# Kernel optimization log

Measured on AMD Instinct MI355X. Metric: run time of the kernel, lower is better.

Reference implementation:

```python
import jax, jax.numpy as jnp
import numpy as np

NUM_HEADS = 12  # from init_kwargs


def setup_inputs() -> dict:
    key = jax.random.key(0)
    k1, k2, k3 = jax.random.split(key, 3)
    B, N, C = 8, 4096, 768
    x = jax.random.normal(k1, (B, N, C), dtype=jnp.float32)
    qkv_w = jax.random.normal(k2, (3 * C, C), dtype=jnp.float32) * (C ** -0.5)
    proj_w = jax.random.normal(k3, (C, C), dtype=jnp.float32) * (C ** -0.5)
    proj_b = jnp.zeros((C,), dtype=jnp.float32)
    return {"x": x, "qkv_w": qkv_w, "proj_w": proj_w, "proj_b": proj_b}


def reference(x, qkv_w, proj_w, proj_b):
    B, N, C = x.shape
    H = NUM_HEADS
    hd = C // H
    h = w = int(round(N ** 0.5))  # spatial grid, N = h*w
    # fused qkv projection (q, k are produced but never consumed, as in source)
    qkv = jnp.einsum('bnc,dc->bnd', x, qkv_w)          # [B, N, 3C]
    qkv = qkv.reshape(B, N, 3, H, hd)
    v = qkv[:, :, 2].transpose(0, 2, 1, 3)             # [B, H, N, hd]
    v2d = v.reshape(B, H, h, w, hd)
    # fft2 over spatial dims; concat(real, imag) then slice[:hd] == real part
    v_real = jnp.fft.fft2(v2d.astype(jnp.float32), axes=(2, 3)).real
    out = v_real.reshape(B, H, N, hd).transpose(0, 2, 1, 3).reshape(B, N, C)
    return jnp.einsum('bnc,dc->bnd', out, proj_w) + proj_b
```

## Files before the change

### kernel.cpp

```cpp
#include <hip/hip_runtime.h>
#include <hip/hip_bf16.h>


typedef __bf16 bf16x8 __attribute__((ext_vector_type(8)));
typedef __bf16 bf16x4 __attribute__((ext_vector_type(4)));
typedef float f32x4 __attribute__((ext_vector_type(4)));
typedef float f32x16 __attribute__((ext_vector_type(16)));
typedef unsigned short ushort_t;
typedef unsigned int uint_t;

typedef __attribute__((address_space(3))) unsigned int lds_u32;
typedef __attribute__((address_space(1))) unsigned int glob_u32;

__device__ __forceinline__ void gl_lds16(const void* g, void* l) {
  __builtin_amdgcn_global_load_lds((const glob_u32*)g, (lds_u32*)l, 16, 0, 0);
}

__device__ __forceinline__ ushort_t f2bf(float f) {
  union { __hip_bfloat16 h; ushort_t s; } cv;
  cv.h = __float2bfloat16(f);
  return cv.s;
}

__device__ __forceinline__ bf16x8 ld_frag(const ushort_t* p) {
  union { bf16x8 v; bf16x4 h[2]; } r;
  r.h[0] = *(const bf16x4*)p;
  r.h[1] = *(const bf16x4*)(p + 4);
  return r.v;
}

__device__ __forceinline__ bf16x8 ld_swz(const ushort_t* rowp, int D0, int sel2) {
  union { bf16x8 v; bf16x4 h[2]; } r;
  r.h[0] = *(const bf16x4*)(rowp + 2 * (D0 ^ sel2));
  r.h[1] = *(const bf16x4*)(rowp + 2 * ((D0 + 2) ^ sel2));
  return r.v;
}

__global__ __launch_bounds__(256) void prep(const float* __restrict__ P,
                                            const float* __restrict__ Q,
                                            ushort_t* __restrict__ TwA,
                                            ushort_t* __restrict__ TwB,
                                            ushort_t* __restrict__ Pb,
                                            ushort_t* __restrict__ Qb) {
  __shared__ ushort_t Ts[4608];
  const int t = threadIdx.x;
  if (blockIdx.x < 7) {
    const int id = blockIdx.x * 256 + t;
    int m, k0, sn;
    ushort_t* out;
    if (id < 768) {
      int r = id % 384, cs = id / 384;
      int l = r & 63, ks = (r >> 6) & 1, mt = r >> 7;
      m = mt * 16 + (l & 15);
      k0 = ks * 32 + (l >> 4) * 8;
      sn = cs;
      out = TwA + id * 8;
    } else {
      int j = id - 768;
      int r = j % 512, cs = j / 512;
      int l = r & 63, ks = (r >> 6) & 1, mt = (r >> 7) & 1, wm = r >> 8;
      m = wm * 32 + mt * 16 + (l & 15);
      k0 = ks * 32 + (l >> 4) * 8;
      sn = cs;
      out = TwB + j * 8;
    }
#pragma unroll
    for (int e = 0; e < 8; ++e) {
      int ph = (m * (k0 + e)) & 63;
      float a = (float)ph * 0.09817477042468104f;
      out[e] = f2bf(sn ? __sinf(a) : __cosf(a));
    }
  } else if (blockIdx.x < 151) {
    const int tile = blockIdx.x - 7;
    const int ti = tile / 12, tj = tile % 12;
    const int r0 = t >> 4, c4 = (t & 15) * 4;
#pragma unroll
    for (int rr = 0; rr < 4; ++rr) {
      const int k = ti * 64 + r0 + rr * 16;
      f32x4 v = *(const f32x4*)&Q[(size_t)(1536 + k) * 768 + tj * 64 + c4];
#pragma unroll
      for (int j = 0; j < 4; ++j)
        Ts[(c4 + j) * 72 + r0 + rr * 16] = f2bf(v[j]);
    }
    __syncthreads();
    const int co = t >> 2, kq = (t & 3) * 16;
    uint4 v0 = *(const uint4*)&Ts[co * 72 + kq];
    uint4 v1 = *(const uint4*)&Ts[co * 72 + kq + 8];
    ushort_t* dst = Qb + (size_t)(tj * 64 + co) * 768 + ti * 64 + kq;
    *(uint4*)&dst[0] = v0;
    *(uint4*)&dst[8] = v1;
  } else {
    const int cid = blockIdx.x - 151;
    const size_t off = (size_t)cid * 2048 + t * 8;
    f32x4 f0 = *(const f32x4*)&P[off];
    f32x4 f1 = *(const f32x4*)&P[off + 4];
    union { ushort_t u[8]; uint4 v; } pk;
#pragma unroll
    for (int j = 0; j < 4; ++j) { pk.u[j] = f2bf(f0[j]); pk.u[4 + j] = f2bf(f1[j]); }
    *(uint4*)&Pb[off] = pk.v;
  }
}

__global__ __launch_bounds__(256) void fft_a_pre(const float* __restrict__ X,
                                                 __hip_bfloat16* __restrict__ Ar,
                                                 __hip_bfloat16* __restrict__ Ai,
                                                 const ushort_t* __restrict__ TwA) {
  __shared__ ushort_t smem[9728];
  ushort_t* Xs = smem;
  ushort_t* Ep = smem;
  const int t = threadIdx.x;
  const int c0 = blockIdx.x * 128;
  const int w = t >> 6, l = t & 63;
  const int lm = l & 15, lq = l >> 4;
  const int s = blockIdx.y;
  const float* src = X + (size_t)s * 64 * 768 + c0;
  const bf16x8* twa = (const bf16x8*)TwA;
  bf16x8 afc[3][2], afs[3][2];
#pragma unroll
  for (int mt = 0; mt < 3; ++mt)
#pragma unroll
    for (int ks = 0; ks < 2; ++ks) {
      afc[mt][ks] = twa[mt * 128 + ks * 64 + l];
      afs[mt][ks] = twa[384 + mt * 128 + ks * 64 + l];
    }
#pragma unroll
  for (int it = 0; it < 4; ++it) {
    const int pr = it * 8 + (t >> 5);
    const int c = (t & 31) * 4;
    const float* rp = src + (size_t)(2 * pr) * 768 + c;
    f32x4 f0 = *(const f32x4*)rp;
    f32x4 f1 = *(const f32x4*)(rp + 768);
#pragma unroll
    for (int j = 0; j < 4; ++j) {
      uint_t pk = (uint_t)f2bf(f0[j]) | ((uint_t)f2bf(f1[j]) << 16);
      const int row = c + j;
      const int d = pr ^ (((row >> 4) & 7) << 1);
      *(uint_t*)&Xs[row * 68 + 2 * d] = pk;
    }
  }
  __syncthreads();
  f32x4 accr[3][2] = {}, acci[3][2] = {};
#pragma unroll
  for (int ks = 0; ks < 2; ++ks) {
    bf16x8 bf[2];
#pragma unroll
    for (int nt = 0; nt < 2; ++nt) {
      int c = w * 32 + nt * 16 + lm;
      int sel2 = ((c >> 4) & 7) << 1;
      bf[nt] = ld_swz(&Xs[c * 68], ks * 16 + lq * 4, sel2);
    }
#pragma unroll
    for (int mt = 0; mt < 3; ++mt)
#pragma unroll
      for (int nt = 0; nt < 2; ++nt) {
        accr[mt][nt] = __builtin_amdgcn_mfma_f32_16x16x32_bf16(afc[mt][ks], bf[nt], accr[mt][nt], 0, 0, 0);
        acci[mt][nt] = __builtin_amdgcn_mfma_f32_16x16x32_bf16(afs[mt][ks], bf[nt], acci[mt][nt], 0, 0, 0);
      }
  }
#pragma unroll
  for (int arr = 0; arr < 2; ++arr) {
    __syncthreads();
#pragma unroll
    for (int mt = 0; mt < 3; ++mt)
#pragma unroll
      for (int nt = 0; nt < 2; ++nt)
#pragma unroll
        for (int r = 0; r < 4; ++r) {
          int row = mt * 16 + lq * 4 + r;
          if (row <= 32) {
            int col = w * 32 + nt * 16 + lm;
            float v = arr ? acci[mt][nt][r] : accr[mt][nt][r];
            Ep[row * 136 + col] = f2bf(v);
          }
        }
    __syncthreads();
    __hip_bfloat16* dst = arr ? Ai : Ar;
#pragma unroll
    for (int it = 0; it < 3; ++it) {
      int idx = it * 256 + t;
      int row = idx >> 4, cq = (idx & 15) * 8;
      if (row <= 32) {
        uint4 v = *(const uint4*)&Ep[row * 136 + cq];
        *(uint4*)&dst[(size_t)(s * 64 + row) * 768 + c0 + cq] = v;
      }
    }
  }
}

__global__ __launch_bounds__(256) void fft_b_mfma(const __hip_bfloat16* __restrict__ Ar,
                                                  const __hip_bfloat16* __restrict__ Ai,
                                                  __hip_bfloat16* __restrict__ Xf,
                                                  const ushort_t* __restrict__ TwB,
                                                  const ushort_t* __restrict__ Pb,
                                                  const ushort_t* __restrict__ Qb,
                                                  __hip_bfloat16* __restrict__ Mb) {
  __shared__ ushort_t smem[17408];
  const int t = threadIdx.x;
  const int w = t >> 6, l = t & 63;

  if (blockIdx.y < 6) {
    ushort_t* As = smem;
    ushort_t* Bs = smem + 8192;
    const int m0 = blockIdx.y * 128;
    const int n0 = blockIdx.x * 128;
    const int wm = w & 1, wn = w >> 1;
    f32x16 acc[2][2] = {};
    const int srow = l >> 3;
    const int schunk = (l & 7) ^ srow;
    const int lr = l & 31, lh = l >> 5;
    for (int kt = 0; kt < 12; ++kt) {
      const int k0 = kt * 64;
#pragma unroll
      for (int i = 0; i < 4; ++i) {
        const int rbase = w * 32 + i * 8;
        const int row = rbase + srow;
        gl_lds16(&Pb[(size_t)(m0 + row) * 768 + k0 + schunk * 8], &As[rbase * 64]);
        gl_lds16(&Qb[(size_t)(n0 + row) * 768 + k0 + schunk * 8], &Bs[rbase * 64]);
      }
      __syncthreads();
#pragma unroll
      for (int ks = 0; ks < 4; ++ks) {
        bf16x8 af[2], bfv[2];
#pragma unroll
        for (int mt = 0; mt < 2; ++mt) {
          int row = wm * 64 + mt * 32 + lr;
          int ch = (ks * 2 + lh) ^ (lr & 7);
          af[mt] = *(const bf16x8*)&As[row * 64 + ch * 8];
        }
#pragma unroll
        for (int nt = 0; nt < 2; ++nt) {
          int row = wn * 64 + nt * 32 + lr;
          int ch = (ks * 2 + lh) ^ (lr & 7);
          bfv[nt] = *(const bf16x8*)&Bs[row * 64 + ch * 8];
        }
#pragma unroll
        for (int mt = 0; mt < 2; ++mt)
#pragma unroll
          for (int nt = 0; nt < 2; ++nt)
            acc[mt][nt] = __builtin_amdgcn_mfma_f32_32x32x16_bf16(af[mt], bfv[nt], acc[mt][nt], 0, 0, 0);
      }
      __syncthreads();
    }
#pragma unroll
    for (int nt = 0; nt < 2; ++nt) {
      const int col = n0 + wn * 64 + nt * 32 + lr;
#pragma unroll
      for (int mt = 0; mt < 2; ++mt) {
        const int rb = m0 + wm * 64 + mt * 32 + 4 * lh;
#pragma unroll
        for (int reg = 0; reg < 16; ++reg) {
          const int row = rb + (reg & 3) + 8 * (reg >> 2);
          Mb[(size_t)row * 768 + col] = __float2bfloat16(acc[mt][nt][reg]);
        }
      }
    }
    return;
  }

  ushort_t* Rs = smem;
  ushort_t* Is = smem + 8704;
  ushort_t* Ep = smem;
  const int bz = blockIdx.y - 6;
  const int b = bz / 33, k2 = bz % 33;
  const int c0 = blockIdx.x * 128;
  const ushort_t* ar = (const ushort_t*)Ar + ((size_t)(b * 64) * 64 + k2) * 768 + c0;
  const ushort_t* ai = (const ushort_t*)Ai + ((size_t)(b * 64) * 64 + k2) * 768 + c0;
  const size_t n1s = (size_t)64 * 768;
  const int wm = w & 1, wn = w >> 1;
  const int lm = l & 15, lq = l >> 4;
  const bf16x8* twb = (const bf16x8*)TwB;
  bf16x8 afc[2][2], afs[2][2];
#pragma unroll
  for (int mt = 0; mt < 2; ++mt)
#pragma unroll
    for (int ks = 0; ks < 2; ++ks) {
      afc[mt][ks] = twb[wm * 256 + mt * 128 + ks * 64 + l];
      afs[mt][ks] = twb[512 + wm * 256 + mt * 128 + ks * 64 + l];
    }
#pragma unroll
  for (int it = 0; it < 4; ++it) {
    const int pr = it * 8 + (t >> 5);
    const int c = (t & 31) * 4;
    const size_t o0 = (size_t)(2 * pr) * n1s + c;
    uint2 va = *(const uint2*)&ar[o0];
    uint2 vb = *(const uint2*)&ar[o0 + n1s];
    uint2 ia = *(const uint2*)&ai[o0];
    uint2 ib = *(const uint2*)&ai[o0 + n1s];
    uint_t rr[4], ss[4];
    rr[0] = (va.x & 0xffffu) | (vb.x << 16);
    rr[1] = (va.x >> 16) | (vb.x & 0xffff0000u);
    rr[2] = (va.y & 0xffffu) | (vb.y << 16);
    rr[3] = (va.y >> 16) | (vb.y & 0xffff0000u);
    ss[0] = (ia.x & 0xffffu) | (ib.x << 16);
    ss[1] = (ia.x >> 16) | (ib.x & 0xffff0000u);
    ss[2] = (ia.y & 0xffffu) | (ib.y << 16);
    ss[3] = (ia.y >> 16) | (ib.y & 0xffff0000u);
#pragma unroll
    for (int j = 0; j < 4; ++j) {
      const int row = c + j;
      const int d = pr ^ (((row >> 4) & 7) << 1);
      *(uint_t*)&Rs[row * 68 + 2 * d] = rr[j];
      *(uint_t*)&Is[row * 68 + 2 * d] = ss[j];
    }
  }
  __syncthreads();
  f32x4 accC[2][4] = {}, accS[2][4] = {};
#pragma unroll
  for (int ks = 0; ks < 2; ++ks) {
    bf16x8 bR[4], bI[4];
#pragma unroll
    for (int nt = 0; nt < 4; ++nt) {
      int c = wn * 64 + nt * 16 + lm;
      int sel2 = ((c >> 4) & 7) << 1;
      int D0 = ks * 16 + lq * 4;
      bR[nt] = ld_swz(&Rs[c * 68], D0, sel2);
      bI[nt] = ld_swz(&Is[c * 68], D0, sel2);
    }
#pragma unroll
    for (int mt = 0; mt < 2; ++mt)
#pragma unroll
      for (int nt = 0; nt < 4; ++nt) {
        accC[mt][nt] = __builtin_amdgcn_mfma_f32_16x16x32_bf16(afc[mt][ks], bR[nt], accC[mt][nt], 0, 0, 0);
        accS[mt][nt] = __builtin_amdgcn_mfma_f32_16x16x32_bf16(afs[mt][ks], bI[nt], accS[mt][nt], 0, 0, 0);
      }
  }
  const int nout = (k2 >= 1 && k2 <= 31) ? 2 : 1;
  for (int o = 0; o < nout; ++o) {
    __syncthreads();
#pragma unroll
    for (int mt = 0; mt < 2; ++mt)
#pragma unroll
      for (int nt = 0; nt < 4; ++nt)
#pragma unroll
        for (int r = 0; r < 4; ++r) {
          int row = wm * 32 + mt * 16 + lq * 4 + r;
          int col = wn * 64 + nt * 16 + lm;
          float v = o ? (accC[mt][nt][r] + accS[mt][nt][r])
                      : (accC[mt][nt][r] - accS[mt][nt][r]);
          Ep[row * 136 + col] = f2bf(v);
        }
    __syncthreads();
    const int k2o = o ? (64 - k2) : k2;
#pragma unroll
    for (int it = 0; it < 4; ++it) {
      int idx = it * 256 + t;
      int k1 = idx >> 4, cq = (idx & 15) * 8;
      uint4 v = *(const uint4*)&Ep[k1 * 136 + cq];
      *(uint4*)&Xf[((size_t)b * 4096 + k1 * 64 + k2o) * 768 + c0 + cq] = v;
    }
  }
}

__global__ __launch_bounds__(256) void gemm_bt(const __hip_bfloat16* __restrict__ A,
                                               const __hip_bfloat16* __restrict__ B,
                                               const float* __restrict__ bias,
                                               float* __restrict__ C) {
  __shared__ ushort_t As[128 * 64];
  __shared__ ushort_t Bs[128 * 64];
  const int t = threadIdx.x, w = t >> 6, l = t & 63;
  const int L = blockIdx.x + blockIdx.y * 6;
  const int s = L >> 3, xcd = L & 7;
  const int n0 = (s % 6) * 128;
  const int m0 = ((s / 6) * 8 + xcd) * 128;
  const int wm = w & 1, wn = w >> 1;
  f32x16 acc[2][2] = {};
  const int srow = l >> 3;
  const int schunk = (l & 7) ^ srow;
  const int lr = l & 31, lh = l >> 5;
  for (int kt = 0; kt < 12; ++kt) {
    const int k0 = kt * 64;
#pragma unroll
    for (int i = 0; i < 4; ++i) {
      const int rbase = w * 32 + i * 8;
      const int row = rbase + srow;
      gl_lds16(&A[(size_t)(m0 + row) * 768 + k0 + schunk * 8], &As[rbase * 64]);
      gl_lds16(&B[(size_t)(n0 + row) * 768 + k0 + schunk * 8], &Bs[rbase * 64]);
    }
    __syncthreads();
#pragma unroll
    for (int ks = 0; ks < 4; ++ks) {
      bf16x8 af[2], bf[2];
#pragma unroll
      for (int mt = 0; mt < 2; ++mt) {
        int row = wm * 64 + mt * 32 + lr;
        int ch = (ks * 2 + lh) ^ (lr & 7);
        af[mt] = *(const bf16x8*)&As[row * 64 + ch * 8];
      }
#pragma unroll
      for (int nt = 0; nt < 2; ++nt) {
        int row = wn * 64 + nt * 32 + lr;
        int ch = (ks * 2 + lh) ^ (lr & 7);
        bf[nt] = *(const bf16x8*)&Bs[row * 64 + ch * 8];
      }
#pragma unroll
      for (int mt = 0; mt < 2; ++mt)
#pragma unroll
        for (int nt = 0; nt < 2; ++nt)
          acc[mt][nt] = __builtin_amdgcn_mfma_f32_32x32x16_bf16(af[mt], bf[nt], acc[mt][nt], 0, 0, 0);
    }
    __syncthreads();
  }
#pragma unroll
  for (int nt = 0; nt < 2; ++nt) {
    const int col = n0 + wn * 64 + nt * 32 + lr;
    const float bv = bias[col];
#pragma unroll
    for (int mt = 0; mt < 2; ++mt) {
      const int rb = m0 + wm * 64 + mt * 32 + 4 * lh;
#pragma unroll
      for (int reg = 0; reg < 16; ++reg) {
        const int row = rb + (reg & 3) + 8 * (reg >> 2);
        C[(size_t)row * 768 + col] = acc[mt][nt][reg] + bv;
      }
    }
  }
}

extern "C" void kernel_launch(void* const* d_in, const int* in_sizes, int n_in,
                              void* d_out, int out_size, void* d_ws, size_t ws_size,
                              hipStream_t stream) {
  const float* x      = (const float*)d_in[0];
  const float* qkv_w  = (const float*)d_in[1];
  const float* proj_w = (const float*)d_in[2];
  const float* proj_b = (const float*)d_in[3];
  float* out = (float*)d_out;

  char* ws = (char*)d_ws;
  const size_t MB_BYTES = (size_t)768 * 768 * 2;
  const size_t ARR_BYTES = (size_t)8 * 4096 * 768 * 2;
  __hip_bfloat16* Mb = (__hip_bfloat16*)ws;
  __hip_bfloat16* Ar = (__hip_bfloat16*)(ws + MB_BYTES);
  __hip_bfloat16* Ai = (__hip_bfloat16*)(ws + MB_BYTES + ARR_BYTES);
  __hip_bfloat16* Xf = (__hip_bfloat16*)(ws + MB_BYTES + 2 * ARR_BYTES);
  ushort_t* Pb = (ushort_t*)(ws + MB_BYTES + 3 * ARR_BYTES);
  ushort_t* Qb = (ushort_t*)(ws + MB_BYTES + 3 * ARR_BYTES + MB_BYTES);
  ushort_t* TwA = (ushort_t*)((char*)Ar + 61440);
  ushort_t* TwB = (ushort_t*)((char*)Ar + 61440 + 12288);

  prep<<<dim3(439), 256, 0, stream>>>(proj_w, qkv_w, TwA, TwB, Pb, Qb);
  fft_a_pre<<<dim3(6, 512), 256, 0, stream>>>(x, Ar, Ai, TwA);
  fft_b_mfma<<<dim3(6, 270), 256, 0, stream>>>(Ar, Ai, Xf, TwB, Pb, Qb, Mb);
  gemm_bt<<<dim3(6, 256), 256, 0, stream>>>(Xf, Mb, proj_b, out);
}
```

Baseline: 255.2 us.

## Process two FFT slices per block in both FFT stages with overlapped epilogue

fft_a_pre now handles two 64-row slices per block, staging both into a doubled LDS buffer and writing real and imaginary outputs in one combined pass. fft_b_mfma pairs columns k2 and k2+16 per block, double-buffering LDS so the second slice's MFMA overlaps the first slice's global stores. The intent is to cut block count, launch and sync overhead and to hide epilogue latency. The cost is twice the LDS per block (about 68KB in fft_b) and more live registers, which lowers occupancy.

After: 252.0 us. About the same (-1.3%).

```diff
diff --git a/kernel.cpp b/kernel.cpp
--- a/kernel.cpp
+++ b/kernel.cpp
@@ -105,15 +105,12 @@
                                                  __hip_bfloat16* __restrict__ Ar,
                                                  __hip_bfloat16* __restrict__ Ai,
                                                  const ushort_t* __restrict__ TwA) {
-  __shared__ ushort_t smem[9728];
-  ushort_t* Xs = smem;
-  ushort_t* Ep = smem;
+  __shared__ ushort_t smem[17408];
   const int t = threadIdx.x;
   const int c0 = blockIdx.x * 128;
   const int w = t >> 6, l = t & 63;
   const int lm = l & 15, lq = l >> 4;
-  const int s = blockIdx.y;
-  const float* src = X + (size_t)s * 64 * 768 + c0;
+  const int s0 = blockIdx.y * 2;
   const bf16x8* twa = (const bf16x8*)TwA;
   bf16x8 afc[3][2], afs[3][2];
 #pragma unroll
@@ -124,64 +121,77 @@
       afs[mt][ks] = twa[384 + mt * 128 + ks * 64 + l];
     }
 #pragma unroll
-  for (int it = 0; it < 4; ++it) {
-    const int pr = it * 8 + (t >> 5);
-    const int c = (t & 31) * 4;
-    const float* rp = src + (size_t)(2 * pr) * 768 + c;
-    f32x4 f0 = *(const f32x4*)rp;
-    f32x4 f1 = *(const f32x4*)(rp + 768);
-#pragma unroll
-    for (int j = 0; j < 4; ++j) {
-      uint_t pk = (uint_t)f2bf(f0[j]) | ((uint_t)f2bf(f1[j]) << 16);
-      const int row = c + j;
-      const int d = pr ^ (((row >> 4) & 7) << 1);
-      *(uint_t*)&Xs[row * 68 + 2 * d] = pk;
+  for (int ss = 0; ss < 2; ++ss) {
+    ushort_t* Xs = smem + ss * 8704;
+    const float* src = X + (size_t)(s0 + ss) * 64 * 768 + c0;
+#pragma unroll
+    for (int it = 0; it < 4; ++it) {
+      const int pr = it * 8 + (t >> 5);
+      const int c = (t & 31) * 4;
+      const float* rp = src + (size_t)(2 * pr) * 768 + c;
+      f32x4 f0 = *(const f32x4*)rp;
+      f32x4 f1 = *(const f32x4*)(rp + 768);
+#pragma unroll
+      for (int j = 0; j < 4; ++j) {
+        uint_t pk = (uint_t)f2bf(f0[j]) | ((uint_t)f2bf(f1[j]) << 16);
+        const int row = c + j;
+        const int d = pr ^ (((row >> 4) & 7) << 1);
+        *(uint_t*)&Xs[row * 68 + 2 * d] = pk;
+      }
     }
   }
   __syncthreads();
-  f32x4 accr[3][2] = {}, acci[3][2] = {};
-#pragma unroll
-  for (int ks = 0; ks < 2; ++ks) {
-    bf16x8 bf[2];
-#pragma unroll
-    for (int nt = 0; nt < 2; ++nt) {
-      int c = w * 32 + nt * 16 + lm;
-      int sel2 = ((c >> 4) & 7) << 1;
-      bf[nt] = ld_swz(&Xs[c * 68], ks * 16 + lq * 4, sel2);
-    }
-#pragma unroll
-    for (int mt = 0; mt < 3; ++mt)
+  f32x4 accr[2][3][2] = {}, acci[2][3][2] = {};
+#pragma unroll
+  for (int ss = 0; ss < 2; ++ss) {
+    const ushort_t* Xs = smem + ss * 8704;
+#pragma unroll
+    for (int ks = 0; ks < 2; ++ks) {
+      bf16x8 bf[2];
 #pragma unroll
       for (int nt = 0; nt < 2; ++nt) {
-        accr[mt][nt] = __builtin_amdgcn_mfma_f32_16x16x32_bf16(afc[mt][ks], bf[nt], accr[mt][nt], 0, 0, 0);
-        acci[mt][nt] = __builtin_amdgcn_mfma_f32_16x16x32_bf16(afs[mt][ks], bf[nt], acci[mt][nt], 0, 0, 0);
-      }
-  }
-#pragma unroll
-  for (int arr = 0; arr < 2; ++arr) {
-    __syncthreads();
-#pragma unroll
-    for (int mt = 0; mt < 3; ++mt)
-#pragma unroll
-      for (int nt = 0; nt < 2; ++nt)
-#pragma unroll
-        for (int r = 0; r < 4; ++r) {
-          int row = mt * 16 + lq * 4 + r;
-          if (row <= 32) {
-            int col = w * 32 + nt * 16 + lm;
-            float v = arr ? acci[mt][nt][r] : accr[mt][nt][r];
-            Ep[row * 136 + col] = f2bf(v);
+        int c = w * 32 + nt * 16 + lm;
+        int sel2 = ((c >> 4) & 7) << 1;
+        bf[nt] = ld_swz(&Xs[c * 68], ks * 16 + lq * 4, sel2);
+      }
+#pragma unroll
+      for (int mt = 0; mt < 3; ++mt)
+#pragma unroll
+        for (int nt = 0; nt < 2; ++nt) {
+          accr[ss][mt][nt] = __builtin_amdgcn_mfma_f32_16x16x32_bf16(afc[mt][ks], bf[nt], accr[ss][mt][nt], 0, 0, 0);
+          acci[ss][mt][nt] = __builtin_amdgcn_mfma_f32_16x16x32_bf16(afs[mt][ks], bf[nt], acci[ss][mt][nt], 0, 0, 0);
+        }
+    }
+  }
+#pragma unroll
+  for (int ss = 0; ss < 2; ++ss) {
+    __syncthreads();
+#pragma unroll
+    for (int arr = 0; arr < 2; ++arr)
+#pragma unroll
+      for (int mt = 0; mt < 3; ++mt)
+#pragma unroll
+        for (int nt = 0; nt < 2; ++nt)
+#pragma unroll
+          for (int r = 0; r < 4; ++r) {
+            int row = mt * 16 + lq * 4 + r;
+            if (row <= 32) {
+              int col = w * 32 + nt * 16 + lm;
+              float v = arr ? acci[ss][mt][nt][r] : accr[ss][mt][nt][r];
+              smem[arr * 6528 + row * 136 + col] = f2bf(v);
+            }
           }
-        }
-    __syncthreads();
-    __hip_bfloat16* dst = arr ? Ai : Ar;
-#pragma unroll
-    for (int it = 0; it < 3; ++it) {
+    __syncthreads();
+#pragma unroll
+    for (int it = 0; it < 5; ++it) {
       int idx = it * 256 + t;
-      int row = idx >> 4, cq = (idx & 15) * 8;
-      if (row <= 32) {
-        uint4 v = *(const uint4*)&Ep[row * 136 + cq];
-        *(uint4*)&dst[(size_t)(s * 64 + row) * 768 + c0 + cq] = v;
+      if (idx < 1056) {
+        int arr = idx >= 528 ? 1 : 0;
+        int rem = idx - arr * 528;
+        int row = rem >> 4, cq = (rem & 15) * 8;
+        uint4 v = *(const uint4*)&smem[arr * 6528 + row * 136 + cq];
+        __hip_bfloat16* dst = arr ? Ai : Ar;
+        *(uint4*)&dst[(size_t)((s0 + ss) * 64 + row) * 768 + c0 + cq] = v;
       }
     }
   }
@@ -194,7 +204,7 @@
                                                   const ushort_t* __restrict__ Pb,
                                                   const ushort_t* __restrict__ Qb,
                                                   __hip_bfloat16* __restrict__ Mb) {
-  __shared__ ushort_t smem[17408];
+  __shared__ ushort_t smem[34816];
   const int t = threadIdx.x;
   const int w = t >> 6, l = t & 63;
 
@@ -257,14 +267,12 @@
     return;
   }
 
-  ushort_t* Rs = smem;
-  ushort_t* Is = smem + 8704;
-  ushort_t* Ep = smem;
   const int bz = blockIdx.y - 6;
-  const int b = bz / 33, k2 = bz % 33;
+  const int b = bz / 17, kp = bz % 17;
+  const int nk = (kp == 16) ? 1 : 2;
+  const int k2v0 = (kp == 16) ? 32 : kp;
+  const int k2v1 = kp + 16;
   const int c0 = blockIdx.x * 128;
-  const ushort_t* ar = (const ushort_t*)Ar + ((size_t)(b * 64) * 64 + k2) * 768 + c0;
-  const ushort_t* ai = (const ushort_t*)Ai + ((size_t)(b * 64) * 64 + k2) * 768 + c0;
   const size_t n1s = (size_t)64 * 768;
   const int wm = w & 1, wn = w >> 1;
   const int lm = l & 15, lq = l >> 4;
@@ -277,77 +285,117 @@
       afc[mt][ks] = twb[wm * 256 + mt * 128 + ks * 64 + l];
       afs[mt][ks] = twb[512 + wm * 256 + mt * 128 + ks * 64 + l];
     }
-#pragma unroll
-  for (int it = 0; it < 4; ++it) {
-    const int pr = it * 8 + (t >> 5);
-    const int c = (t & 31) * 4;
-    const size_t o0 = (size_t)(2 * pr) * n1s + c;
-    uint2 va = *(const uint2*)&ar[o0];
-    uint2 vb = *(const uint2*)&ar[o0 + n1s];
-    uint2 ia = *(const uint2*)&ai[o0];
-    uint2 ib = *(const uint2*)&ai[o0 + n1s];
-    uint_t rr[4], ss[4];
-    rr[0] = (va.x & 0xffffu) | (vb.x << 16);
-    rr[1] = (va.x >> 16) | (vb.x & 0xffff0000u);
-    rr[2] = (va.y & 0xffffu) | (vb.y << 16);
-    rr[3] = (va.y >> 16) | (vb.y & 0xffff0000u);
-    ss[0] = (ia.x & 0xffffu) | (ib.x << 16);
-    ss[1] = (ia.x >> 16) | (ib.x & 0xffff0000u);
-    ss[2] = (ia.y & 0xffffu) | (ib.y << 16);
-    ss[3] = (ia.y >> 16) | (ib.y & 0xffff0000u);
-#pragma unroll
-    for (int j = 0; j < 4; ++j) {
-      const int row = c + j;
-      const int d = pr ^ (((row >> 4) & 7) << 1);
-      *(uint_t*)&Rs[row * 68 + 2 * d] = rr[j];
-      *(uint_t*)&Is[row * 68 + 2 * d] = ss[j];
-    }
-  }
+
+  auto stage = [&](int kk, int k2) {
+    ushort_t* Rs = smem + kk * 17408;
+    ushort_t* Is = Rs + 8704;
+    const ushort_t* ar = (const ushort_t*)Ar + ((size_t)(b * 64) * 64 + k2) * 768 + c0;
+    const ushort_t* ai = (const ushort_t*)Ai + ((size_t)(b * 64) * 64 + k2) * 768 + c0;
+#pragma unroll
+    for (int it = 0; it < 4; ++it) {
+      const int pr = it * 8 + (t >> 5);
+      const int c = (t & 31) * 4;
+      const size_t o0 = (size_t)(2 * pr) * n1s + c;
+      uint2 va = *(const uint2*)&ar[o0];
+      uint2 vb = *(const uint2*)&ar[o0 + n1s];
+      uint2 ia = *(const uint2*)&ai[o0];
+      uint2 ib = *(const uint2*)&ai[o0 + n1s];
+      uint_t rr[4], ss_[4];
+      rr[0] = (va.x & 0xffffu) | (vb.x << 16);
+      rr[1] = (va.x >> 16) | (vb.x & 0xffff0000u);
+      rr[2] = (va.y & 0xffffu) | (vb.y << 16);
+      rr[3] = (va.y >> 16) | (vb.y & 0xffff0000u);
+      ss_[0] = (ia.x & 0xffffu) | (ib.x << 16);
+      ss_[1] = (ia.x >> 16) | (ib.x & 0xffff0000u);
+      ss_[2] = (ia.y & 0xffffu) | (ib.y << 16);
+      ss_[3] = (ia.y >> 16) | (ib.y & 0xffff0000u);
+#pragma unroll
+      for (int j = 0; j < 4; ++j) {
+        const int row = c + j;
+        const int d = pr ^ (((row >> 4) & 7) << 1);
+        *(uint_t*)&Rs[row * 68 + 2 * d] = rr[j];
+        *(uint_t*)&Is[row * 68 + 2 * d] = ss_[j];
+      }
+    }
+  };
+
+  auto do_mfma = [&](int kk, f32x4 (&aC)[2][4], f32x4 (&aS)[2][4]) {
+    const ushort_t* Rs = smem + kk * 17408;
+    const ushort_t* Is = Rs + 8704;
+#pragma unroll
+    for (int ks = 0; ks < 2; ++ks) {
+      bf16x8 bR[4], bI[4];
+#pragma unroll
+      for (int nt = 0; nt < 4; ++nt) {
+        int c = wn * 64 + nt * 16 + lm;
+        int sel2 = ((c >> 4) & 7) << 1;
+        int D0 = ks * 16 + lq * 4;
+        bR[nt] = ld_swz(&Rs[c * 68], D0, sel2);
+        bI[nt] = ld_swz(&Is[c * 68], D0, sel2);
+      }
+#pragma unroll
+      for (int mt = 0; mt < 2; ++mt)
+#pragma unroll
+        for (int nt = 0; nt < 4; ++nt) {
+          aC[mt][nt] = __builtin_amdgcn_mfma_f32_16x16x32_bf16(afc[mt][ks], bR[nt], aC[mt][nt], 0, 0, 0);
+          aS[mt][nt] = __builtin_amdgcn_mfma_f32_16x16x32_bf16(afs[mt][ks], bI[nt], aS[mt][nt], 0, 0, 0);
+        }
+    }
+  };
+
+  auto ep_write = [&](int kk, int nout, f32x4 (&aC)[2][4], f32x4 (&aS)[2][4]) {
+    ushort_t* Ep = smem + kk * 17408;
+    for (int o = 0; o < nout; ++o)
+#pragma unroll
+      for (int mt = 0; mt < 2; ++mt)
+#pragma unroll
+        for (int nt = 0; nt < 4; ++nt)
+#pragma unroll
+          for (int r = 0; r < 4; ++r) {
+            int row = wm * 32 + mt * 16 + lq * 4 + r;
+            int col = wn * 64 + nt * 16 + lm;
+            float v = o ? (aC[mt][nt][r] + aS[mt][nt][r])
+                        : (aC[mt][nt][r] - aS[mt][nt][r]);
+            Ep[o * 8704 + row * 136 + col] = f2bf(v);
+          }
+  };
+
+  auto gout = [&](int kk, int k2, int nout) {
+    const ushort_t* Ep = smem + kk * 17408;
+#pragma unroll
+    for (int it = 0; it < 8; ++it) {
+      int idx = it * 256 + t;
+      if (idx < nout * 1024) {
+        int o = idx >> 10, rem = idx & 1023;
+        int k1 = rem >> 4, cq = (rem & 15) * 8;
+        uint4 v = *(const uint4*)&Ep[o * 8704 + k1 * 136 + cq];
+        int k2o = o ? (64 - k2) : k2;
+        *(uint4*)&Xf[((size_t)b * 4096 + k1 * 64 + k2o) * 768 + c0 + cq] = v;
+      }
+    }
+  };
+
+  const int nout0 = (k2v0 >= 1 && k2v0 <= 31) ? 2 : 1;
+  stage(0, k2v0);
+  if (nk == 2) stage(1, k2v1);
   __syncthreads();
-  f32x4 accC[2][4] = {}, accS[2][4] = {};
-#pragma unroll
-  for (int ks = 0; ks < 2; ++ks) {
-    bf16x8 bR[4], bI[4];
-#pragma unroll
-    for (int nt = 0; nt < 4; ++nt) {
-      int c = wn * 64 + nt * 16 + lm;
-      int sel2 = ((c >> 4) & 7) << 1;
-      int D0 = ks * 16 + lq * 4;
-      bR[nt] = ld_swz(&Rs[c * 68], D0, sel2);
-      bI[nt] = ld_swz(&Is[c * 68], D0, sel2);
-    }
-#pragma unroll
-    for (int mt = 0; mt < 2; ++mt)
-#pragma unroll
-      for (int nt = 0; nt < 4; ++nt) {
-        accC[mt][nt] = __builtin_amdgcn_mfma_f32_16x16x32_bf16(afc[mt][ks], bR[nt], accC[mt][nt], 0, 0, 0);
-        accS[mt][nt] = __builtin_amdgcn_mfma_f32_16x16x32_bf16(afs[mt][ks], bI[nt], accS[mt][nt], 0, 0, 0);
-      }
-  }
-  const int nout = (k2 >= 1 && k2 <= 31) ? 2 : 1;
-  for (int o = 0; o < nout; ++o) {
-    __syncthreads();
-#pragma unroll
-    for (int mt = 0; mt < 2; ++mt)
-#pragma unroll
-      for (int nt = 0; nt < 4; ++nt)
-#pragma unroll
-        for (int r = 0; r < 4; ++r) {
-          int row = wm * 32 + mt * 16 + lq * 4 + r;
-          int col = wn * 64 + nt * 16 + lm;
-          float v = o ? (accC[mt][nt][r] + accS[mt][nt][r])
-                      : (accC[mt][nt][r] - accS[mt][nt][r]);
-          Ep[row * 136 + col] = f2bf(v);
-        }
-    __syncthreads();
-    const int k2o = o ? (64 - k2) : k2;
-#pragma unroll
-    for (int it = 0; it < 4; ++it) {
-      int idx = it * 256 + t;
-      int k1 = idx >> 4, cq = (idx & 15) * 8;
-      uint4 v = *(const uint4*)&Ep[k1 * 136 + cq];
-      *(uint4*)&Xf[((size_t)b * 4096 + k1 * 64 + k2o) * 768 + c0 + cq] = v;
-    }
+  {
+    f32x4 aC[2][4] = {}, aS[2][4] = {};
+    do_mfma(0, aC, aS);
+    __syncthreads();
+    ep_write(0, nout0, aC, aS);
+  }
+  __syncthreads();
+  if (nk == 2) {
+    f32x4 aC[2][4] = {}, aS[2][4] = {};
+    do_mfma(1, aC, aS);
+    gout(0, k2v0, nout0);
+    __syncthreads();
+    ep_write(1, 2, aC, aS);
+    __syncthreads();
+    gout(1, k2v1, 2);
+  } else {
+    gout(0, k2v0, nout0);
   }
 }
 
@@ -438,7 +486,7 @@
   ushort_t* TwB = (ushort_t*)((char*)Ar + 61440 + 12288);
 
   prep<<<dim3(439), 256, 0, stream>>>(proj_w, qkv_w, TwA, TwB, Pb, Qb);
-  fft_a_pre<<<dim3(6, 512), 256, 0, stream>>>(x, Ar, Ai, TwA);
-  fft_b_mfma<<<dim3(6, 270), 256, 0, stream>>>(Ar, Ai, Xf, TwB, Pb, Qb, Mb);
+  fft_a_pre<<<dim3(6, 256), 256, 0, stream>>>(x, Ar, Ai, TwA);
+  fft_b_mfma<<<dim3(6, 142), 256, 0, stream>>>(Ar, Ai, Xf, TwB, Pb, Qb, Mb);
   gemm_bt<<<dim3(6, 256), 256, 0, stream>>>(Xf, Mb, proj_b, out);
 }
```

## Compact intermediate FFT arrays to k2-major layout and merge epilogue syncs

Applied to the files above, without the earlier changes.

Stores the first-stage FFT outputs Ar/Ai in a packed [b][k2][n1] layout of 33 rows instead of strided 64-row slots. The second stage then reads contiguous 768-wide rows rather than rows strided by 64*768. Both FFT kernels now stage both epilogue outputs in shared memory at once and write them after a single barrier instead of looping with two barriers per output. Twiddle buffers move to their own workspace region. The aim is better read locality and coalescing, a smaller intermediate footprint and fewer barriers, at the cost of more shared memory live at the same time.

New measurement: 253.1 us. About the same (-0.8%).

```diff
diff --git a/kernel.cpp b/kernel.cpp
--- a/kernel.cpp
+++ b/kernel.cpp
@@ -20,13 +20,6 @@
   union { __hip_bfloat16 h; ushort_t s; } cv;
   cv.h = __float2bfloat16(f);
   return cv.s;
-}
-
-__device__ __forceinline__ bf16x8 ld_frag(const ushort_t* p) {
-  union { bf16x8 v; bf16x4 h[2]; } r;
-  r.h[0] = *(const bf16x4*)p;
-  r.h[1] = *(const bf16x4*)(p + 4);
-  return r.v;
 }
 
 __device__ __forceinline__ bf16x8 ld_swz(const ushort_t* rowp, int D0, int sel2) {
@@ -106,13 +99,12 @@
                                                  __hip_bfloat16* __restrict__ Ai,
                                                  const ushort_t* __restrict__ TwA) {
   __shared__ ushort_t smem[9728];
-  ushort_t* Xs = smem;
-  ushort_t* Ep = smem;
   const int t = threadIdx.x;
   const int c0 = blockIdx.x * 128;
   const int w = t >> 6, l = t & 63;
   const int lm = l & 15, lq = l >> 4;
   const int s = blockIdx.y;
+  const int b = s >> 6, n1 = s & 63;
   const float* src = X + (size_t)s * 64 * 768 + c0;
   const bf16x8* twa = (const bf16x8*)TwA;
   bf16x8 afc[3][2], afs[3][2];
@@ -135,7 +127,7 @@
       uint_t pk = (uint_t)f2bf(f0[j]) | ((uint_t)f2bf(f1[j]) << 16);
       const int row = c + j;
       const int d = pr ^ (((row >> 4) & 7) << 1);
-      *(uint_t*)&Xs[row * 68 + 2 * d] = pk;
+      *(uint_t*)&smem[row * 68 + 2 * d] = pk;
     }
   }
   __syncthreads();
@@ -147,7 +139,7 @@
     for (int nt = 0; nt < 2; ++nt) {
       int c = w * 32 + nt * 16 + lm;
       int sel2 = ((c >> 4) & 7) << 1;
-      bf[nt] = ld_swz(&Xs[c * 68], ks * 16 + lq * 4, sel2);
+      bf[nt] = ld_swz(&smem[c * 68], ks * 16 + lq * 4, sel2);
     }
 #pragma unroll
     for (int mt = 0; mt < 3; ++mt)
@@ -157,9 +149,9 @@
         acci[mt][nt] = __builtin_amdgcn_mfma_f32_16x16x32_bf16(afs[mt][ks], bf[nt], acci[mt][nt], 0, 0, 0);
       }
   }
-#pragma unroll
-  for (int arr = 0; arr < 2; ++arr) {
-    __syncthreads();
+  __syncthreads();
+#pragma unroll
+  for (int arr = 0; arr < 2; ++arr)
 #pragma unroll
     for (int mt = 0; mt < 3; ++mt)
 #pragma unroll
@@ -170,19 +162,20 @@
           if (row <= 32) {
             int col = w * 32 + nt * 16 + lm;
             float v = arr ? acci[mt][nt][r] : accr[mt][nt][r];
-            Ep[row * 136 + col] = f2bf(v);
+            smem[arr * 4488 + row * 136 + col] = f2bf(v);
           }
         }
-    __syncthreads();
-    __hip_bfloat16* dst = arr ? Ai : Ar;
-#pragma unroll
-    for (int it = 0; it < 3; ++it) {
-      int idx = it * 256 + t;
-      int row = idx >> 4, cq = (idx & 15) * 8;
-      if (row <= 32) {
-        uint4 v = *(const uint4*)&Ep[row * 136 + cq];
-        *(uint4*)&dst[(size_t)(s * 64 + row) * 768 + c0 + cq] = v;
-      }
+  __syncthreads();
+#pragma unroll
+  for (int it = 0; it < 5; ++it) {
+    int idx = it * 256 + t;
+    if (idx < 1056) {
+      int arr = idx >= 528 ? 1 : 0;
+      int rem = idx - arr * 528;
+      int row = rem >> 4, cq = (rem & 15) * 8;
+      uint4 v = *(const uint4*)&smem[arr * 4488 + row * 136 + cq];
+      __hip_bfloat16* dst = arr ? Ai : Ar;
+      *(uint4*)&dst[((size_t)(b * 33 + row) * 64 + n1) * 768 + c0 + cq] = v;
     }
   }
 }
@@ -259,13 +252,11 @@
 
   ushort_t* Rs = smem;
   ushort_t* Is = smem + 8704;
-  ushort_t* Ep = smem;
   const int bz = blockIdx.y - 6;
   const int b = bz / 33, k2 = bz % 33;
   const int c0 = blockIdx.x * 128;
-  const ushort_t* ar = (const ushort_t*)Ar + ((size_t)(b * 64) * 64 + k2) * 768 + c0;
-  const ushort_t* ai = (const ushort_t*)Ai + ((size_t)(b * 64) * 64 + k2) * 768 + c0;
-  const size_t n1s = (size_t)64 * 768;
+  const ushort_t* ar = (const ushort_t*)Ar + (size_t)(b * 33 + k2) * 64 * 768 + c0;
+  const ushort_t* ai = (const ushort_t*)Ai + (size_t)(b * 33 + k2) * 64 * 768 + c0;
   const int wm = w & 1, wn = w >> 1;
   const int lm = l & 15, lq = l >> 4;
   const bf16x8* twb = (const bf16x8*)TwB;
@@ -281,26 +272,26 @@
   for (int it = 0; it < 4; ++it) {
     const int pr = it * 8 + (t >> 5);
     const int c = (t & 31) * 4;
-    const size_t o0 = (size_t)(2 * pr) * n1s + c;
+    const size_t o0 = (size_t)(2 * pr) * 768 + c;
     uint2 va = *(const uint2*)&ar[o0];
-    uint2 vb = *(const uint2*)&ar[o0 + n1s];
+    uint2 vb = *(const uint2*)&ar[o0 + 768];
     uint2 ia = *(const uint2*)&ai[o0];
-    uint2 ib = *(const uint2*)&ai[o0 + n1s];
-    uint_t rr[4], ss[4];
+    uint2 ib = *(const uint2*)&ai[o0 + 768];
+    uint_t rr[4], ss_[4];
     rr[0] = (va.x & 0xffffu) | (vb.x << 16);
     rr[1] = (va.x >> 16) | (vb.x & 0xffff0000u);
     rr[2] = (va.y & 0xffffu) | (vb.y << 16);
     rr[3] = (va.y >> 16) | (vb.y & 0xffff0000u);
-    ss[0] = (ia.x & 0xffffu) | (ib.x << 16);
-    ss[1] = (ia.x >> 16) | (ib.x & 0xffff0000u);
-    ss[2] = (ia.y & 0xffffu) | (ib.y << 16);
-    ss[3] = (ia.y >> 16) | (ib.y & 0xffff0000u);
+    ss_[0] = (ia.x & 0xffffu) | (ib.x << 16);
+    ss_[1] = (ia.x >> 16) | (ib.x & 0xffff0000u);
+    ss_[2] = (ia.y & 0xffffu) | (ib.y << 16);
+    ss_[3] = (ia.y >> 16) | (ib.y & 0xffff0000u);
 #pragma unroll
     for (int j = 0; j < 4; ++j) {
       const int row = c + j;
       const int d = pr ^ (((row >> 4) & 7) << 1);
       *(uint_t*)&Rs[row * 68 + 2 * d] = rr[j];
-      *(uint_t*)&Is[row * 68 + 2 * d] = ss[j];
+      *(uint_t*)&Is[row * 68 + 2 * d] = ss_[j];
     }
   }
   __syncthreads();
@@ -325,8 +316,8 @@
       }
   }
   const int nout = (k2 >= 1 && k2 <= 31) ? 2 : 1;
-  for (int o = 0; o < nout; ++o) {
-    __syncthreads();
+  __syncthreads();
+  for (int o = 0; o < nout; ++o)
 #pragma unroll
     for (int mt = 0; mt < 2; ++mt)
 #pragma unroll
@@ -337,15 +328,17 @@
           int col = wn * 64 + nt * 16 + lm;
           float v = o ? (accC[mt][nt][r] + accS[mt][nt][r])
                       : (accC[mt][nt][r] - accS[mt][nt][r]);
-          Ep[row * 136 + col] = f2bf(v);
+          smem[o * 8704 + row * 136 + col] = f2bf(v);
         }
-    __syncthreads();
-    const int k2o = o ? (64 - k2) : k2;
-#pragma unroll
-    for (int it = 0; it < 4; ++it) {
-      int idx = it * 256 + t;
-      int k1 = idx >> 4, cq = (idx & 15) * 8;
-      uint4 v = *(const uint4*)&Ep[k1 * 136 + cq];
+  __syncthreads();
+#pragma unroll
+  for (int it = 0; it < 8; ++it) {
+    int idx = it * 256 + t;
+    if (idx < nout * 1024) {
+      int o = idx >> 10, rem = idx & 1023;
+      int k1 = rem >> 4, cq = (rem & 15) * 8;
+      uint4 v = *(const uint4*)&smem[o * 8704 + k1 * 136 + cq];
+      int k2o = o ? (64 - k2) : k2;
       *(uint4*)&Xf[((size_t)b * 4096 + k1 * 64 + k2o) * 768 + c0 + cq] = v;
     }
   }
@@ -427,15 +420,16 @@
 
   char* ws = (char*)d_ws;
   const size_t MB_BYTES = (size_t)768 * 768 * 2;
-  const size_t ARR_BYTES = (size_t)8 * 4096 * 768 * 2;
+  const size_t AK_BYTES = (size_t)8 * 33 * 64 * 768 * 2;
+  const size_t XF_BYTES = (size_t)8 * 4096 * 768 * 2;
   __hip_bfloat16* Mb = (__hip_bfloat16*)ws;
   __hip_bfloat16* Ar = (__hip_bfloat16*)(ws + MB_BYTES);
-  __hip_bfloat16* Ai = (__hip_bfloat16*)(ws + MB_BYTES + ARR_BYTES);
-  __hip_bfloat16* Xf = (__hip_bfloat16*)(ws + MB_BYTES + 2 * ARR_BYTES);
-  ushort_t* Pb = (ushort_t*)(ws + MB_BYTES + 3 * ARR_BYTES);
-  ushort_t* Qb = (ushort_t*)(ws + MB_BYTES + 3 * ARR_BYTES + MB_BYTES);
-  ushort_t* TwA = (ushort_t*)((char*)Ar + 61440);
-  ushort_t* TwB = (ushort_t*)((char*)Ar + 61440 + 12288);
+  __hip_bfloat16* Ai = (__hip_bfloat16*)(ws + MB_BYTES + AK_BYTES);
+  __hip_bfloat16* Xf = (__hip_bfloat16*)(ws + MB_BYTES + 2 * AK_BYTES);
+  ushort_t* Pb  = (ushort_t*)(ws + MB_BYTES + 2 * AK_BYTES + XF_BYTES);
+  ushort_t* Qb  = (ushort_t*)((char*)Pb + MB_BYTES);
+  ushort_t* TwA = (ushort_t*)((char*)Qb + MB_BYTES);
+  ushort_t* TwB = (ushort_t*)((char*)TwA + 12288);
 
   prep<<<dim3(439), 256, 0, stream>>>(proj_w, qkv_w, TwA, TwB, Pb, Qb);
   fft_a_pre<<<dim3(6, 512), 256, 0, stream>>>(x, Ar, Ai, TwA);
```
